# Optimization experiments

Measured on AMD Instinct MI355X. Metric: run time of the kernel, lower is better.

The kernel has to match this reference:

```python
import jax, jax.numpy as jnp
import numpy as np

H = 1024   # lstm hidden size
F = 512    # feature dim
P = 66     # pose dim
T_IN = 10
T_OUT = 25


def _glorot(key, shape):
    fan = shape[-1]
    return jax.random.normal(key, shape, dtype=jnp.float32) / np.sqrt(fan)


def setup_inputs() -> dict:
    key = jax.random.key(0)
    ks = jax.random.split(key, 24)
    B = 256
    inp = {
        'x': jax.random.normal(ks[0], (B, T_IN, P), dtype=jnp.float32),
        'z': jax.random.normal(ks[1], (B, T_IN, P), dtype=jnp.float32),
        'for_resid': jax.random.normal(ks[2], (B, T_OUT, P), dtype=jnp.float32),
        # ToFeature: Linear(66 -> 512)
        'tf_w': _glorot(ks[3], (F, P)), 'tf_b': jnp.zeros((F,), jnp.float32),
        # encoder LSTM(512 -> 1024)
        'enc_wih': _glorot(ks[4], (4 * H, F)), 'enc_whh': _glorot(ks[5], (4 * H, H)),
        'enc_bih': jnp.zeros((4 * H,), jnp.float32), 'enc_bhh': jnp.zeros((4 * H,), jnp.float32),
        # encoder_post LSTM(512 -> 1024)
        'encp_wih': _glorot(ks[6], (4 * H, F)), 'encp_whh': _glorot(ks[7], (4 * H, H)),
        'encp_bih': jnp.zeros((4 * H,), jnp.float32), 'encp_bhh': jnp.zeros((4 * H,), jnp.float32),
        # decoder cell LSTM(512 -> 1024)
        'dec_wih': _glorot(ks[8], (4 * H, F)), 'dec_whh': _glorot(ks[9], (4 * H, H)),
        'dec_bih': jnp.zeros((4 * H,), jnp.float32), 'dec_bhh': jnp.zeros((4 * H,), jnp.float32),
        # decoder lin: Linear(1024 -> 512)
        'lin_w': _glorot(ks[10], (F, H)), 'lin_b': jnp.zeros((F,), jnp.float32),
        # ToPose: Linear(1024 -> 66)
        'tp_w': _glorot(ks[11], (P, H)), 'tp_b': jnp.zeros((P,), jnp.float32),
    }
    return inp


def _lstm_step(h, c, xt, wih, whh, bih, bhh):
    gates = xt @ wih.T + bih + h @ whh.T + bhh  # (B, 4H)
    i, f, g, o = jnp.split(gates, 4, axis=-1)
    c_new = jax.nn.sigmoid(f) * c + jax.nn.sigmoid(i) * jnp.tanh(g)
    h_new = jax.nn.sigmoid(o) * jnp.tanh(c_new)
    return h_new, c_new


def _lstm_scan(xs, wih, whh, bih, bhh):
    # xs: (T, B, I)
    B = xs.shape[1]
    h0 = jnp.zeros((B, H), xs.dtype)
    c0 = jnp.zeros((B, H), xs.dtype)

    def step(carry, xt):
        h, c = carry
        h, c = _lstm_step(h, c, xt, wih, whh, bih, bhh)
        return (h, c), h

    (h_n, c_n), all_h = jax.lax.scan(step, (h0, c0), xs)
    return all_h, h_n, c_n


def reference(x, z, for_resid, tf_w, tf_b,
              enc_wih, enc_whh, enc_bih, enc_bhh,
              encp_wih, encp_whh, encp_bih, encp_bhh,
              dec_wih, dec_whh, dec_bih, dec_bhh,
              lin_w, lin_b, tp_w, tp_b):
    # ToFeature + permute to time-major (T, B, F)
    xf = jnp.transpose(x @ tf_w.T + tf_b, (1, 0, 2))
    zf = jnp.transpose(z @ tf_w.T + tf_b, (1, 0, 2))

    all_h, h_n, c_n = _lstm_scan(xf, enc_wih, enc_whh, enc_bih, enc_bhh)   # (10,B,H)
    all_hz, _, _ = _lstm_scan(zf, encp_wih, encp_whh, encp_bih, encp_bhh)  # (10,B,H)

    def dec_step(carry, _):
        h, c = carry                                   # (B,H), (B,H)
        cat_h = jnp.concatenate([all_h, h[None], all_hz], axis=0)  # (21,B,H)
        scores = jnp.einsum('bh,tbh->tb', c, cat_h)
        attw = jax.nn.softmax(scores, axis=0)
        atth = jnp.einsum('tb,tbh->bh', attw, cat_h)   # attention context -> LSTM h0
        inp = h @ lin_w.T + lin_b                      # (B,F)
        h_new, c_new = _lstm_step(atth, c, inp, dec_wih, dec_whh, dec_bih, dec_bhh)
        return (h_new, c_new), h_new

    _, dec_hs = jax.lax.scan(dec_step, (h_n, c_n), None, length=T_OUT)  # (25,B,H)
    out = jnp.transpose(dec_hs, (1, 0, 2))             # (B,25,H)
    o = out @ tp_w.T + tp_b                            # (B,25,66)
    return o + for_resid
```

## Files before the change

### kernel.cpp

```cpp
#include <hip/hip_runtime.h>
#include <hip/hip_bf16.h>
#include <hip/hip_cooperative_groups.h>

namespace cg = cooperative_groups;

#define DEV __device__ __forceinline__

typedef unsigned short u16;
typedef short bf16x8_t __attribute__((ext_vector_type(8)));
typedef float f32x4_t __attribute__((ext_vector_type(4)));

constexpr int NBLK = 256;
constexpr int NTHR = 512;
constexpr int NT_ALL = NBLK * NTHR;
constexpr size_t HSTRIDE = 256 * 1024;

struct Params {
  const float *x, *z, *resid, *tf_w, *tf_b;
  const float *e_wih, *e_whh, *e_bih, *e_bhh;
  const float *p_wih, *p_whh, *p_bih, *p_bhh;
  const float *d_wih, *d_whh, *d_bih, *d_bhh;
  const float *lin_w, *lin_b, *tp_w, *tp_b;
  u16 *Wenc, *Wencp, *Wdec, *wihP, *linT, *tpw;
  float *bias_e, *bias_ep, *bias_d, *bias_part;
  u16 *xf, *zf;
  u16 *he, *hp;
  u16 *hs;
  u16 *atth;
  float *c_pub;
  unsigned *bar;
  float *out;
};

DEV float b2f(u16 v) { unsigned u = ((unsigned)v) << 16; float f; __builtin_memcpy(&f, &u, 4); return f; }
DEV u16 f2b(float f) {
  unsigned u; __builtin_memcpy(&u, &f, 4);
  unsigned r = u + 0x7fffu + ((u >> 16) & 1u);
  return (u16)(r >> 16);
}
DEV unsigned pk2(float a, float b) { return (unsigned)f2b(a) | ((unsigned)f2b(b) << 16); }
DEV uint4 cvt8(const float* s) {
  float4 a = *(const float4*)s;
  float4 b = *(const float4*)(s + 4);
  uint4 r;
  r.x = pk2(a.x, a.y); r.y = pk2(a.z, a.w);
  r.z = pk2(b.x, b.y); r.w = pk2(b.z, b.w);
  return r;
}
DEV float sigm(float x) { return 1.0f / (1.0f + __expf(-x)); }
DEV f32x4_t fzero4() { f32x4_t v = {0.f, 0.f, 0.f, 0.f}; return v; }

DEV void gll16(const void* g, void* l) {
  __builtin_amdgcn_global_load_lds(
      (const __attribute__((address_space(1))) void*)g,
      (__attribute__((address_space(3))) void*)l, 16, 0, 0);
}

template <typename T> DEV void st_wt(T* p, T v) {
  __hip_atomic_store(p, v, __ATOMIC_RELAXED, __HIP_MEMORY_SCOPE_AGENT);
}
template <typename T> DEV T ld_byp(const T* p) {
  return __hip_atomic_load(p, __ATOMIC_RELAXED, __HIP_MEMORY_SCOPE_AGENT);
}

DEV void gridbar(unsigned* ctrs, unsigned ep, int tid, int bid) {
  asm volatile("s_waitcnt vmcnt(0)" ::: "memory");
  __syncthreads();
  if (tid == 0) atomicAdd(&ctrs[(bid & 7) * 16], 1u);
  if (tid < 8) {
    const unsigned tgt = ep * 32u;
    while (ld_byp(&ctrs[tid * 16]) < tgt) __builtin_amdgcn_s_sleep(2);
  }
  __syncthreads();
}
DEV void lanebar(unsigned* ctrs, unsigned ep, int lane, int j, int tid) {
  asm volatile("s_waitcnt vmcnt(0)" ::: "memory");
  __syncthreads();
  if (tid == 0) atomicAdd(&ctrs[(8 + lane * 2 + (j & 1)) * 16], 1u);
  if (tid < 2) {
    const unsigned tgt = ep * 32u;
    while (ld_byp(&ctrs[(8 + lane * 2 + tid) * 16]) < tgt) __builtin_amdgcn_s_sleep(1);
  }
  __syncthreads();
}

template <int PM>
DEV void gemm64(const u16* __restrict__ xa, int ldx, int xcols,
                const u16* __restrict__ ha, int ldh,
                const u16* __restrict__ wsrc, int ldw, int K,
                int m0, int n0, int tid, char* sm, f32x4_t acc[2]) {
  char* lB = sm;
  char* lA = sm + 32768;
  const int NK = K >> 6;
  const int row = tid >> 3, uu = tid & 7;
  const int usw = uu ^ (row & 7);
  const int wv = tid >> 6;
  char* la_base = lA + (wv << 10);
  char* lb_base = lB + (wv << 10);

  auto stageA = [&](int ks) {
    const int k0 = ks << 6;
    const u16* ga;
    if (k0 < xcols) ga = xa + (size_t)(m0 + row) * ldx + (k0 + usw * 8);
    else            ga = ha + (size_t)(m0 + row) * ldh + (k0 - xcols + usw * 8);
    gll16(ga, la_base + ((ks & 3) << 13));
  };
  auto stageB = [&](int ks) {
    const int k0 = ks << 6;
    const u16* gb = wsrc + (size_t)(n0 + row) * ldw + (k0 + usw * 8);
    gll16(gb, lb_base + ((ks & 3) << 13));
  };

  const int l = tid & 63, l15 = l & 15, lhi = l >> 4;
  const int wr = wv >> 1, wc = wv & 1;
  const int rA = wr * 16 + l15;
  const int aoff0 = rA * 128 + ((lhi ^ (rA & 7)) << 4);
  const int aoff1 = rA * 128 + (((lhi + 4) ^ (rA & 7)) << 4);
  const int nB0 = wc * 32 + l15, nB1 = nB0 + 16;
  const int boff00 = nB0 * 128 + ((lhi ^ (nB0 & 7)) << 4);
  const int boff01 = nB0 * 128 + (((lhi + 4) ^ (nB0 & 7)) << 4);
  const int boff10 = nB1 * 128 + ((lhi ^ (nB1 & 7)) << 4);
  const int boff11 = nB1 * 128 + (((lhi + 4) ^ (nB1 & 7)) << 4);

  if (PM == 0) { stageA(0); stageB(0); stageA(1); stageB(1); }
  if (PM == 2) { stageA(0); stageA(1); }

#pragma unroll 1
  for (int ks = 0; ks < NK; ++ks) {
    if (ks + 2 < NK) { stageA(ks + 2); stageB(ks + 2); }
    if (ks == 0)            asm volatile("s_waitcnt vmcnt(3)" ::: "memory");
    else if (ks + 2 < NK)   asm volatile("s_waitcnt vmcnt(4)" ::: "memory");
    else if (ks + 2 == NK)  asm volatile("s_waitcnt vmcnt(2)" ::: "memory");
    else                    asm volatile("s_waitcnt vmcnt(0)" ::: "memory");
    __builtin_amdgcn_s_barrier();
    const char* A  = lA + ((ks & 3) << 13);
    const char* Bb = lB + ((ks & 3) << 13);
    bf16x8_t a0  = *(const bf16x8_t*)(A + aoff0);
    bf16x8_t a1  = *(const bf16x8_t*)(A + aoff1);
    bf16x8_t b00 = *(const bf16x8_t*)(Bb + boff00);
    bf16x8_t b01 = *(const bf16x8_t*)(Bb + boff01);
    bf16x8_t b10 = *(const bf16x8_t*)(Bb + boff10);
    bf16x8_t b11 = *(const bf16x8_t*)(Bb + boff11);
    acc[0] = __builtin_amdgcn_mfma_f32_16x16x32_bf16(a0, b00, acc[0], 0, 0, 0);
    acc[0] = __builtin_amdgcn_mfma_f32_16x16x32_bf16(a1, b01, acc[0], 0, 0, 0);
    acc[1] = __builtin_amdgcn_mfma_f32_16x16x32_bf16(a0, b10, acc[1], 0, 0, 0);
    acc[1] = __builtin_amdgcn_mfma_f32_16x16x32_bf16(a1, b11, acc[1], 0, 0, 0);
  }
  __builtin_amdgcn_s_barrier();
}

DEV void pre_slotAB(const u16* xa, int ldx, int xcols, const u16* ha, int ldh,
                    const u16* wsrc, int ldw, int m0, int n0, int tid, char* sm,
                    int ks) {
  char* lB = sm; char* lA = sm + 32768;
  const int row = tid >> 3, uu = tid & 7;
  const int usw = uu ^ (row & 7);
  const int wv = tid >> 6;
  const int k0 = ks << 6;
  const u16* ga;
  if (k0 < xcols) ga = xa + (size_t)(m0 + row) * ldx + (k0 + usw * 8);
  else            ga = ha + (size_t)(m0 + row) * ldh + (k0 - xcols + usw * 8);
  const u16* gb = wsrc + (size_t)(n0 + row) * ldw + (k0 + usw * 8);
  gll16(ga, lA + (wv << 10) + ((ks & 3) << 13));
  gll16(gb, lB + (wv << 10) + ((ks & 3) << 13));
}
DEV void pre_slotB(const u16* wsrc, int ldw, int n0, int tid, char* sm, int ks) {
  char* lB = sm;
  const int row = tid >> 3, uu = tid & 7;
  const int usw = uu ^ (row & 7);
  const int wv = tid >> 6;
  const int k0 = ks << 6;
  const u16* gb = wsrc + (size_t)(n0 + row) * ldw + (k0 + usw * 8);
  gll16(gb, lB + (wv << 10) + ((ks & 3) << 13));
}

DEV void lstm_ep_reg(const f32x4_t acc[2], int tid, char* sm,
                     const float* __restrict__ bias, float cc[2],
                     u16* __restrict__ hw, float* __restrict__ cpub,
                     int m0, int n0) {
  float* gl = (float*)(sm + 49152);
  const int l = tid & 63, l15 = l & 15, lhi = l >> 4;
  const int wv = tid >> 6, wr = wv >> 1, wc = wv & 1;
#pragma unroll
  for (int j = 0; j < 2; ++j)
#pragma unroll
    for (int qq = 0; qq < 4; ++qq)
      gl[(wr * 16 + lhi * 4 + qq) * 64 + wc * 32 + j * 16 + l15] = acc[j][qq];
  __syncthreads();
#pragma unroll
  for (int it = 0; it < 2; ++it) {
    int idx = it * 512 + tid;
    int r = idx >> 4, jj = idx & 15;
    f32x4_t g4 = *(const f32x4_t*)(gl + r * 64 + jj * 4);
    f32x4_t b4 = *(const f32x4_t*)(bias + n0 + jj * 4);
    float ig = sigm(g4[0] + b4[0]);
    float fg = sigm(g4[1] + b4[1]);
    float g_ = tanhf(g4[2] + b4[2]);
    float og = sigm(g4[3] + b4[3]);
    float cn = fg * cc[it] + ig * g_;
    cc[it] = cn;
    float hn = og * tanhf(cn);
    size_t off = (size_t)(m0 + r) * 1024 + (n0 >> 2) + jj;
    st_wt(&hw[off], f2b(hn));
    if (cpub) st_wt(&cpub[off], cn);
  }
  __syncthreads();
}

DEV void wx_store(const f32x4_t acc[2], int tid, u16* __restrict__ Wdec,
                  int m0, int n0) {
  const int l = tid & 63, l15 = l & 15, lhi = l >> 4;
  const int wv = tid >> 6, wr = wv >> 1, wc = wv & 1;
#pragma unroll
  for (int j = 0; j < 2; ++j)
#pragma unroll
    for (int qq = 0; qq < 4; ++qq) {
      int r = m0 + wr * 16 + lhi * 4 + qq;
      int c = n0 + wc * 32 + j * 16 + l15;
      st_wt(&Wdec[(size_t)r * 2048 + c], f2b(acc[j][qq]));
    }
}

DEV void phase0_tf(const Params& p, int bid, int tid, char* sm) {
  float* xs = (float*)sm;
  float* zs = (float*)(sm + 2688);
  for (int g = tid; g < 660; g += NTHR) {
    int t = g / 66, q = g - t * 66;
    xs[g] = p.x[((size_t)bid * 10 + t) * 66 + q];
    zs[g] = p.z[((size_t)bid * 10 + t) * 66 + q];
  }
  __syncthreads();
  const int n = tid;
  float accx[10], accz[10];
  float bn = p.tf_b[n];
#pragma unroll
  for (int t = 0; t < 10; ++t) { accx[t] = bn; accz[t] = bn; }
  const float* wrow = p.tf_w + (size_t)n * 66;
  for (int k = 0; k < 66; ++k) {
    float wk = wrow[k];
#pragma unroll
    for (int t = 0; t < 10; ++t) {
      accx[t] = fmaf(wk, xs[t * 66 + k], accx[t]);
      accz[t] = fmaf(wk, zs[t * 66 + k], accz[t]);
    }
  }
#pragma unroll
  for (int t = 0; t < 10; ++t) {
    p.xf[(size_t)t * 131072 + (size_t)bid * 512 + n] = f2b(accx[t]);
    p.zf[(size_t)t * 131072 + (size_t)bid * 512 + n] = f2b(accz[t]);
  }
  __syncthreads();
}

DEV void phase0a(const Params& p, int gtid) {
  for (int g = gtid; g < 786432; g += NT_ALL) {
    int row = g / 192;
    int u = g - row * 192;
    int k = u * 8;
    int nsrc = (row & 3) * 1024 + (row >> 2);
    const float* s1 = (k < 512) ? (p.e_wih + (size_t)nsrc * 512 + k)
                                : (p.e_whh + (size_t)nsrc * 1024 + (k - 512));
    ((uint4*)p.Wenc)[g] = cvt8(s1);
    const float* s2 = (k < 512) ? (p.p_wih + (size_t)nsrc * 512 + k)
                                : (p.p_whh + (size_t)nsrc * 1024 + (k - 512));
    ((uint4*)p.Wencp)[g] = cvt8(s2);
  }
  for (int g = gtid; g < 524288; g += NT_ALL) {
    int row = g >> 7, u = g & 127;
    int nsrc = (row & 3) * 1024 + (row >> 2);
    ((uint4*)p.Wdec)[row * 256 + 128 + u] = cvt8(p.d_whh + (size_t)nsrc * 1024 + u * 8);
  }
  for (int g = gtid; g < 262144; g += NT_ALL) {
    int row = g >> 6, u = g & 63;
    int nsrc = (row & 3) * 1024 + (row >> 2);
    ((uint4*)p.wihP)[g] = cvt8(p.d_wih + (size_t)nsrc * 512 + u * 8);
  }
  for (int g = gtid; g < 524288; g += NT_ALL) {
    int f = g >> 10, h = g & 1023;
    p.linT[(size_t)h * 512 + f] = f2b(p.lin_w[g]);
  }
  for (int g = gtid; g < 8448; g += NT_ALL)
    ((uint4*)p.tpw)[g] = cvt8(p.tp_w + g * 8);
  for (int g = gtid; g < 4096; g += NT_ALL) {
    int nsrc = (g & 3) * 1024 + (g >> 2);
    p.bias_e[g]  = p.e_bih[nsrc] + p.e_bhh[nsrc];
    p.bias_ep[g] = p.p_bih[nsrc] + p.p_bhh[nsrc];
  }
  for (int g = gtid; g < 32768; g += NT_ALL) {
    int cell = g >> 3, sub = g & 7;
    int nsrc = (cell & 3) * 1024 + (cell >> 2);
    const float* wr_ = p.d_wih + (size_t)nsrc * 512 + sub * 64;
    const float* lb = p.lin_b + sub * 64;
    float s = 0.f;
    for (int f = 0; f < 64; ++f) s += wr_[f] * lb[f];
    p.bias_part[g] = s;
  }
  uint4 zz; zz.x = zz.y = zz.z = zz.w = 0u;
  for (int g = gtid; g < 32768; g += NT_ALL) { ((uint4*)p.he)[g] = zz; ((uint4*)p.hp)[g] = zz; }
}

DEV void attention(const Params& p, const u16* hd_prev, const float* cpub,
                   u16* atth_s, int b, int tid, char* sm) {
  u16*   catl = (u16*)(sm + 16384);
  float* cl   = (float*)(sm + 59392);
  float* sc   = (float*)(sm + 63488);
  for (int g = tid; g < 2688; g += NTHR) {
    int t = g >> 7, hu = g & 127;
    const u16* src;
    if (t < 10)       src = p.he + (size_t)(t + 1) * HSTRIDE;
    else if (t == 10) src = hd_prev;
    else              src = p.hp + (size_t)(t - 10) * HSTRIDE;
    ((uint4*)catl)[g] = *(const uint4*)(src + (size_t)b * 1024 + hu * 8);
  }
  for (int g = tid; g < 512; g += NTHR) {
    unsigned long long v = ld_byp(((const unsigned long long*)(cpub + (size_t)b * 1024)) + g);
    ((unsigned long long*)cl)[g] = v;
  }
  __syncthreads();
  const int wv = tid >> 6, l = tid & 63;
  for (int t = wv; t < 21; t += 8) {
    float s = 0.f;
    const u16* cr = catl + t * 1024;
    for (int hh = l; hh < 1024; hh += 64) s += cl[hh] * b2f(cr[hh]);
#pragma unroll
    for (int o = 32; o; o >>= 1) s += __shfl_down(s, o);
    if (l == 0) sc[t] = s;
  }
  __syncthreads();
  float m = -1e30f;
#pragma unroll
  for (int t = 0; t < 21; ++t) m = fmaxf(m, sc[t]);
  float e[21]; float den = 0.f;
#pragma unroll
  for (int t = 0; t < 21; ++t) { e[t] = __expf(sc[t] - m); den += e[t]; }
  float inv = 1.0f / den;
  const int h0 = tid * 2;
  float a0 = 0.f, a1 = 0.f;
#pragma unroll
  for (int t = 0; t < 21; ++t) {
    float w_ = e[t] * inv;
    unsigned v = *(const unsigned*)(catl + t * 1024 + h0);
    a0 += w_ * b2f((u16)(v & 0xffff));
    a1 += w_ * b2f((u16)(v >> 16));
  }
  st_wt(((unsigned*)(atth_s + (size_t)b * 1024)) + tid, pk2(a0, a1));
  __syncthreads();
}

DEV void finalproj(const Params& p, int b, int tid, char* sm) {
  u16* hl = (u16*)sm;
  for (int g = tid; g < 3200; g += NTHR) {
    int t = g >> 7, hu = g & 127;
    ((uint4*)hl)[g] = *(const uint4*)(p.hs + ((size_t)(t * 256 + b)) * 1024 + hu * 8);
  }
  __syncthreads();
  if (tid < 330) {
    int pcol = tid % 66, tg = tid / 66;
    float acc[5] = {0.f, 0.f, 0.f, 0.f, 0.f};
    const u16* wrow = p.tpw + (size_t)pcol * 1024;
    for (int hc = 0; hc < 128; ++hc) {
      uint4 wv4 = ((const uint4*)wrow)[hc];
      float wf[8];
      wf[0] = b2f(wv4.x & 0xffff); wf[1] = b2f(wv4.x >> 16);
      wf[2] = b2f(wv4.y & 0xffff); wf[3] = b2f(wv4.y >> 16);
      wf[4] = b2f(wv4.z & 0xffff); wf[5] = b2f(wv4.z >> 16);
      wf[6] = b2f(wv4.w & 0xffff); wf[7] = b2f(wv4.w >> 16);
#pragma unroll
      for (int r = 0; r < 5; ++r) {
        int t = tg * 5 + r;
        uint4 hv = ((const uint4*)(hl + t * 1024))[hc];
        float s;
        s  = wf[0] * b2f(hv.x & 0xffff) + wf[1] * b2f(hv.x >> 16);
        s += wf[2] * b2f(hv.y & 0xffff) + wf[3] * b2f(hv.y >> 16);
        s += wf[4] * b2f(hv.z & 0xffff) + wf[5] * b2f(hv.z >> 16);
        s += wf[6] * b2f(hv.w & 0xffff) + wf[7] * b2f(hv.w >> 16);
        acc[r] += s;
      }
    }
    float bb = p.tp_b[pcol];
#pragma unroll
    for (int r = 0; r < 5; ++r) {
      int t = tg * 5 + r;
      size_t o = (size_t)b * 1650 + (size_t)t * 66 + pcol;
      p.out[o] = acc[r] + bb + p.resid[o];
    }
  }
}

__global__ __launch_bounds__(NTHR) void model_kernel(Params p) {
  cg::grid_group gg = cg::this_grid();
  __shared__ __align__(16) char sm[65536];
  const int tid = threadIdx.x;
  const int bid = blockIdx.x;
  const int gtid = bid * NTHR + tid;

  phase0_tf(p, bid, tid, sm);
  phase0a(p, gtid);
  if (bid == 0 && tid < 16) st_wt(&p.bar[tid * 16], 0u);
  gg.sync();

  for (int g = gtid; g < 4096; g += NT_ALL) {
    int nsrc = (g & 3) * 1024 + (g >> 2);
    float s = p.d_bih[nsrc] + p.d_bhh[nsrc];
#pragma unroll
    for (int k8 = 0; k8 < 8; ++k8) s += p.bias_part[g * 8 + k8];
    st_wt(&p.bias_d[g], s);
  }
#pragma unroll 1
  for (int i = 0; i < 4; ++i) {
    int tt = bid * 4 + i;
    int m0w = (tt & 63) << 6;
    int n0w = (tt >> 6) << 6;
    f32x4_t acc[2]; acc[0] = fzero4(); acc[1] = fzero4();
    gemm64<0>(p.wihP, 512, 512, p.wihP, 0, p.linT, 512, 512, m0w, n0w, tid, sm, acc);
    wx_store(acc, tid, p.Wdec, m0w, n0w);
  }

  const int lane = bid >> 6, j = bid & 63;
  const int m0 = lane << 6;
  const int n0 = ((j & 7) * 8 + (j >> 3)) << 6;
  const int b = (lane << 6) + j;

  pre_slotAB(p.xf, 512, 512, p.he, 1024, p.Wenc, 1536, m0, n0, tid, sm, 0);
  pre_slotAB(p.xf, 512, 512, p.he, 1024, p.Wenc, 1536, m0, n0, tid, sm, 1);
  gridbar(p.bar, 1, tid, bid);

  float ce[2] = {0.f, 0.f}, cp[2] = {0.f, 0.f};
  unsigned lep = 0;

#pragma unroll 1
  for (int t = 0; t < 10; ++t) {
    f32x4_t acc[2]; acc[0] = fzero4(); acc[1] = fzero4();
    gemm64<1>(p.xf + (size_t)t * 131072, 512, 512, p.he + (size_t)t * HSTRIDE, 1024,
              p.Wenc, 1536, 1536, m0, n0, tid, sm, acc);
    pre_slotAB(p.zf + (size_t)t * 131072, 512, 512, p.hp, 1024, p.Wencp, 1536, m0, n0, tid, sm, 0);
    pre_slotAB(p.zf + (size_t)t * 131072, 512, 512, p.hp, 1024, p.Wencp, 1536, m0, n0, tid, sm, 1);
    lstm_ep_reg(acc, tid, sm, p.bias_e, ce, p.he + (size_t)(t + 1) * HSTRIDE,
                (t == 9) ? p.c_pub : (float*)0, m0, n0);
    acc[0] = fzero4(); acc[1] = fzero4();
    gemm64<1>(p.zf + (size_t)t * 131072, 512, 512, p.hp + (size_t)t * HSTRIDE, 1024,
              p.Wencp, 1536, 1536, m0, n0, tid, sm, acc);
    if (t < 9) {
      pre_slotAB(p.xf + (size_t)(t + 1) * 131072, 512, 512, p.he, 1024, p.Wenc, 1536, m0, n0, tid, sm, 0);
      pre_slotAB(p.xf + (size_t)(t + 1) * 131072, 512, 512, p.he, 1024, p.Wenc, 1536, m0, n0, tid, sm, 1);
    } else {
      pre_slotB(p.Wdec, 2048, n0, tid, sm, 0);
      pre_slotB(p.Wdec, 2048, n0, tid, sm, 1);
    }
    lstm_ep_reg(acc, tid, sm, p.bias_ep, cp, p.hp + (size_t)(t + 1) * HSTRIDE,
                (float*)0, m0, n0);
    ++lep; lanebar(p.bar, lep, lane, j, tid);
  }

#pragma unroll 1
  for (int s = 0; s < 25; ++s) {
    const u16* hd_prev = (s == 0) ? (p.he + (size_t)10 * HSTRIDE)
                                  : (p.hs + (size_t)(s - 1) * HSTRIDE);
    u16* atth_s = p.atth + (size_t)s * HSTRIDE;
    attention(p, hd_prev, p.c_pub + (size_t)(s & 1) * 262144, atth_s, b, tid, sm);
    f32x4_t acc[2]; acc[0] = fzero4(); acc[1] = fzero4();
    gemm64<2>(hd_prev, 1024, 1024, hd_prev, 1024, p.Wdec, 2048, 1024,
              m0, n0, tid, sm, acc);
    pre_slotB(p.Wdec + 1024, 2048, n0, tid, sm, 0);
    pre_slotB(p.Wdec + 1024, 2048, n0, tid, sm, 1);
    ++lep; lanebar(p.bar, lep, lane, j, tid);
    gemm64<2>(atth_s, 1024, 1024, atth_s, 1024, p.Wdec + 1024, 2048, 1024,
              m0, n0, tid, sm, acc);
    lstm_ep_reg(acc, tid, sm, p.bias_d, ce, p.hs + (size_t)s * HSTRIDE,
                p.c_pub + (size_t)((s + 1) & 1) * 262144, m0, n0);
    if (s < 24) {
      pre_slotB(p.Wdec, 2048, n0, tid, sm, 0);
      pre_slotB(p.Wdec, 2048, n0, tid, sm, 1);
    }
    ++lep; lanebar(p.bar, lep, lane, j, tid);
  }

  finalproj(p, b, tid, sm);
}

extern "C" void kernel_launch(void* const* d_in, const int* in_sizes, int n_in,
                              void* d_out, int out_size, void* d_ws, size_t ws_size,
                              hipStream_t stream) {
  (void)in_sizes; (void)n_in; (void)out_size;
  Params P;
  P.x     = (const float*)d_in[0];
  P.z     = (const float*)d_in[1];
  P.resid = (const float*)d_in[2];
  P.tf_w  = (const float*)d_in[3];
  P.tf_b  = (const float*)d_in[4];
  P.e_wih = (const float*)d_in[5];
  P.e_whh = (const float*)d_in[6];
  P.e_bih = (const float*)d_in[7];
  P.e_bhh = (const float*)d_in[8];
  P.p_wih = (const float*)d_in[9];
  P.p_whh = (const float*)d_in[10];
  P.p_bih = (const float*)d_in[11];
  P.p_bhh = (const float*)d_in[12];
  P.d_wih = (const float*)d_in[13];
  P.d_whh = (const float*)d_in[14];
  P.d_bih = (const float*)d_in[15];
  P.d_bhh = (const float*)d_in[16];
  P.lin_w = (const float*)d_in[17];
  P.lin_b = (const float*)d_in[18];
  P.tp_w  = (const float*)d_in[19];
  P.tp_b  = (const float*)d_in[20];

  char* w = (char*)d_ws;
  size_t o = 0;
  auto take = [&](size_t bytes) { char* r = w + o; o = (o + bytes + 255) & ~(size_t)255; return r; };
  P.Wenc  = (u16*)take(4096ull * 1536 * 2);
  P.Wencp = (u16*)take(4096ull * 1536 * 2);
  P.Wdec  = (u16*)take(4096ull * 2048 * 2);
  P.wihP  = (u16*)take(4096ull * 512 * 2);
  P.linT  = (u16*)take(1024ull * 512 * 2);
  P.tpw   = (u16*)take(66ull * 1024 * 2);
  P.bias_e    = (float*)take(4096 * 4);
  P.bias_ep   = (float*)take(4096 * 4);
  P.bias_d    = (float*)take(4096 * 4);
  P.bias_part = (float*)take(32768 * 4);
  P.xf  = (u16*)take(10ull * 256 * 512 * 2);
  P.zf  = (u16*)take(10ull * 256 * 512 * 2);
  P.he  = (u16*)take(11ull * 256 * 1024 * 2);
  P.hp  = (u16*)take(11ull * 256 * 1024 * 2);
  P.hs  = (u16*)take(25ull * 256 * 1024 * 2);
  P.atth = (u16*)take(25ull * 256 * 1024 * 2);
  P.c_pub = (float*)take(2ull * 256 * 1024 * 4);
  P.bar = (unsigned*)take(16 * 64);
  P.out = (float*)d_out;

  if (o > ws_size) return;

  void* args[] = { &P };
  hipLaunchCooperativeKernel((const void*)model_kernel, dim3(NBLK, 1, 1),
                             dim3(NTHR, 1, 1), args, 0, stream);
}
```

Measured before the change: 815.1 us.

## Load weight tiles directly into registers and stage only activations through LDS

The GEMM now loads the weight (B) fragments straight from global memory into registers with an even/odd double buffer, and stages only the activation (A) operand through LDS. The cross-phase weight prefetches into LDS are removed, and lane barriers now spread arrivals over 8 counters instead of 2. LDS becomes dynamic with a padded epilogue layout. This is meant to cut LDS traffic and barrier contention, but it loses the prefetch overlap across phases and adds register pressure.

```diff
diff --git a/kernel.cpp b/kernel.cpp
--- a/kernel.cpp
+++ b/kernel.cpp
@@ -14,6 +14,7 @@
 constexpr int NTHR = 512;
 constexpr int NT_ALL = NBLK * NTHR;
 constexpr size_t HSTRIDE = 256 * 1024;
+constexpr int SMEM_BYTES = 86016;
 
 struct Params {
   const float *x, *z, *resid, *tf_w, *tf_b;
@@ -63,135 +64,114 @@
   return __hip_atomic_load(p, __ATOMIC_RELAXED, __HIP_MEMORY_SCOPE_AGENT);
 }
 
-DEV void gridbar(unsigned* ctrs, unsigned ep, int tid, int bid) {
+DEV void fullbar(unsigned* ctrs, int bid, unsigned tgt, int tid) {
   asm volatile("s_waitcnt vmcnt(0)" ::: "memory");
   __syncthreads();
   if (tid == 0) atomicAdd(&ctrs[(bid & 7) * 16], 1u);
-  if (tid < 8) {
-    const unsigned tgt = ep * 32u;
-    while (ld_byp(&ctrs[tid * 16]) < tgt) __builtin_amdgcn_s_sleep(2);
-  }
-  __syncthreads();
-}
-DEV void lanebar(unsigned* ctrs, unsigned ep, int lane, int j, int tid) {
+  if (tid < 8) { while (ld_byp(&ctrs[tid * 16]) < tgt) __builtin_amdgcn_s_sleep(2); }
+  __syncthreads();
+}
+DEV void lanebar8(unsigned* ctrs, int lane, int j, unsigned tgt, int tid) {
   asm volatile("s_waitcnt vmcnt(0)" ::: "memory");
   __syncthreads();
-  if (tid == 0) atomicAdd(&ctrs[(8 + lane * 2 + (j & 1)) * 16], 1u);
-  if (tid < 2) {
-    const unsigned tgt = ep * 32u;
-    while (ld_byp(&ctrs[(8 + lane * 2 + tid) * 16]) < tgt) __builtin_amdgcn_s_sleep(1);
-  }
-  __syncthreads();
-}
-
-template <int PM>
-DEV void gemm64(const u16* __restrict__ xa, int ldx, int xcols,
-                const u16* __restrict__ ha, int ldh,
-                const u16* __restrict__ wsrc, int ldw, int K,
-                int m0, int n0, int tid, char* sm, f32x4_t acc[2]) {
-  char* lB = sm;
-  char* lA = sm + 32768;
+  if (tid == 0) atomicAdd(&ctrs[(8 + lane * 8 + (j & 7)) * 16], 1u);
+  if (tid < 8) { while (ld_byp(&ctrs[(8 + lane * 8 + tid) * 16]) < tgt) __builtin_amdgcn_s_sleep(1); }
+  __syncthreads();
+}
+
+struct Bpre { bf16x8_t e00, e01, e10, e11, o00, o01, o10, o11; };
+
+DEV void gemmT(const u16* __restrict__ xa, int ldx, int xcols,
+               const u16* __restrict__ ha, int ldh,
+               const u16* __restrict__ w, int ldw, int K,
+               int m0, int n0, int tid, char* sm, f32x4_t acc[2]) {
+  Bpre B;
   const int NK = K >> 6;
-  const int row = tid >> 3, uu = tid & 7;
-  const int usw = uu ^ (row & 7);
-  const int wv = tid >> 6;
-  char* la_base = lA + (wv << 10);
-  char* lb_base = lB + (wv << 10);
-
-  auto stageA = [&](int ks) {
-    const int k0 = ks << 6;
-    const u16* ga;
-    if (k0 < xcols) ga = xa + (size_t)(m0 + row) * ldx + (k0 + usw * 8);
-    else            ga = ha + (size_t)(m0 + row) * ldh + (k0 - xcols + usw * 8);
-    gll16(ga, la_base + ((ks & 3) << 13));
-  };
-  auto stageB = [&](int ks) {
-    const int k0 = ks << 6;
-    const u16* gb = wsrc + (size_t)(n0 + row) * ldw + (k0 + usw * 8);
-    gll16(gb, lb_base + ((ks & 3) << 13));
-  };
-
-  const int l = tid & 63, l15 = l & 15, lhi = l >> 4;
-  const int wr = wv >> 1, wc = wv & 1;
-  const int rA = wr * 16 + l15;
+  const int row = tid >> 3, usw8 = ((tid & 7) ^ (row & 7)) * 8, wv = tid >> 6;
+  char* dst = sm + (wv << 10);
+  const u16* aX = xa + (size_t)(m0 + row) * ldx + usw8;
+  const u16* aH = ha + (size_t)(m0 + row) * ldh + usw8 - xcols;
+  const int wc = (tid >> 6) & 1, l15 = tid & 15, lhi = (tid & 63) >> 4;
+  const u16* pb0 = w + (size_t)(n0 + wc * 32 + l15) * ldw + lhi * 8;
+  const u16* pb1 = pb0 + (size_t)16 * ldw;
+  const int rA = (tid >> 7) * 16 + l15;
   const int aoff0 = rA * 128 + ((lhi ^ (rA & 7)) << 4);
   const int aoff1 = rA * 128 + (((lhi + 4) ^ (rA & 7)) << 4);
-  const int nB0 = wc * 32 + l15, nB1 = nB0 + 16;
-  const int boff00 = nB0 * 128 + ((lhi ^ (nB0 & 7)) << 4);
-  const int boff01 = nB0 * 128 + (((lhi + 4) ^ (nB0 & 7)) << 4);
-  const int boff10 = nB1 * 128 + ((lhi ^ (nB1 & 7)) << 4);
-  const int boff11 = nB1 * 128 + (((lhi + 4) ^ (nB1 & 7)) << 4);
-
-  if (PM == 0) { stageA(0); stageB(0); stageA(1); stageB(1); }
-  if (PM == 2) { stageA(0); stageA(1); }
-
+
+  auto sA = [&](int ks) {
+    const int k0 = ks << 6;
+    const u16* g = (k0 < xcols) ? (aX + k0) : (aH + k0);
+    gll16(g, dst + ((ks & 3) << 13));
+  };
+  auto ldE = [&](int ks) {
+    const int k0 = ks << 6;
+    B.e00 = *(const bf16x8_t*)(pb0 + k0);
+    B.e01 = *(const bf16x8_t*)(pb0 + k0 + 32);
+    B.e10 = *(const bf16x8_t*)(pb1 + k0);
+    B.e11 = *(const bf16x8_t*)(pb1 + k0 + 32);
+  };
+  auto ldO = [&](int ks) {
+    const int k0 = ks << 6;
+    B.o00 = *(const bf16x8_t*)(pb0 + k0);
+    B.o01 = *(const bf16x8_t*)(pb0 + k0 + 32);
+    B.o10 = *(const bf16x8_t*)(pb1 + k0);
+    B.o11 = *(const bf16x8_t*)(pb1 + k0 + 32);
+  };
+
+  sA(0); ldE(0); sA(1); ldO(1);
+
+  auto body = [&](int ks, bool useE, int wN, bool issue) {
+    if (wN == 5) asm volatile("s_waitcnt vmcnt(5)" ::: "memory");
+    else         asm volatile("s_waitcnt vmcnt(0)" ::: "memory");
+    __builtin_amdgcn_sched_barrier(0);
+    __builtin_amdgcn_s_barrier();
+    __builtin_amdgcn_sched_barrier(0);
+    const char* Asl = sm + ((ks & 3) << 13);
+    bf16x8_t a0 = *(const bf16x8_t*)(Asl + aoff0);
+    bf16x8_t a1 = *(const bf16x8_t*)(Asl + aoff1);
+    if (useE) {
+      acc[0] = __builtin_amdgcn_mfma_f32_16x16x32_bf16(a0, B.e00, acc[0], 0, 0, 0);
+      acc[0] = __builtin_amdgcn_mfma_f32_16x16x32_bf16(a1, B.e01, acc[0], 0, 0, 0);
+      acc[1] = __builtin_amdgcn_mfma_f32_16x16x32_bf16(a0, B.e10, acc[1], 0, 0, 0);
+      acc[1] = __builtin_amdgcn_mfma_f32_16x16x32_bf16(a1, B.e11, acc[1], 0, 0, 0);
+    } else {
+      acc[0] = __builtin_amdgcn_mfma_f32_16x16x32_bf16(a0, B.o00, acc[0], 0, 0, 0);
+      acc[0] = __builtin_amdgcn_mfma_f32_16x16x32_bf16(a1, B.o01, acc[0], 0, 0, 0);
+      acc[1] = __builtin_amdgcn_mfma_f32_16x16x32_bf16(a0, B.o10, acc[1], 0, 0, 0);
+      acc[1] = __builtin_amdgcn_mfma_f32_16x16x32_bf16(a1, B.o11, acc[1], 0, 0, 0);
+    }
+    if (issue) { sA(ks + 2); if (useE) ldE(ks + 2); else ldO(ks + 2); }
+  };
+
+  body(0, true, 5, true);
+  body(1, false, 5, true);
 #pragma unroll 1
-  for (int ks = 0; ks < NK; ++ks) {
-    if (ks + 2 < NK) { stageA(ks + 2); stageB(ks + 2); }
-    if (ks == 0)            asm volatile("s_waitcnt vmcnt(3)" ::: "memory");
-    else if (ks + 2 < NK)   asm volatile("s_waitcnt vmcnt(4)" ::: "memory");
-    else if (ks + 2 == NK)  asm volatile("s_waitcnt vmcnt(2)" ::: "memory");
-    else                    asm volatile("s_waitcnt vmcnt(0)" ::: "memory");
-    __builtin_amdgcn_s_barrier();
-    const char* A  = lA + ((ks & 3) << 13);
-    const char* Bb = lB + ((ks & 3) << 13);
-    bf16x8_t a0  = *(const bf16x8_t*)(A + aoff0);
-    bf16x8_t a1  = *(const bf16x8_t*)(A + aoff1);
-    bf16x8_t b00 = *(const bf16x8_t*)(Bb + boff00);
-    bf16x8_t b01 = *(const bf16x8_t*)(Bb + boff01);
-    bf16x8_t b10 = *(const bf16x8_t*)(Bb + boff10);
-    bf16x8_t b11 = *(const bf16x8_t*)(Bb + boff11);
-    acc[0] = __builtin_amdgcn_mfma_f32_16x16x32_bf16(a0, b00, acc[0], 0, 0, 0);
-    acc[0] = __builtin_amdgcn_mfma_f32_16x16x32_bf16(a1, b01, acc[0], 0, 0, 0);
-    acc[1] = __builtin_amdgcn_mfma_f32_16x16x32_bf16(a0, b10, acc[1], 0, 0, 0);
-    acc[1] = __builtin_amdgcn_mfma_f32_16x16x32_bf16(a1, b11, acc[1], 0, 0, 0);
-  }
-  __builtin_amdgcn_s_barrier();
-}
-
-DEV void pre_slotAB(const u16* xa, int ldx, int xcols, const u16* ha, int ldh,
-                    const u16* wsrc, int ldw, int m0, int n0, int tid, char* sm,
-                    int ks) {
-  char* lB = sm; char* lA = sm + 32768;
-  const int row = tid >> 3, uu = tid & 7;
-  const int usw = uu ^ (row & 7);
-  const int wv = tid >> 6;
-  const int k0 = ks << 6;
-  const u16* ga;
-  if (k0 < xcols) ga = xa + (size_t)(m0 + row) * ldx + (k0 + usw * 8);
-  else            ga = ha + (size_t)(m0 + row) * ldh + (k0 - xcols + usw * 8);
-  const u16* gb = wsrc + (size_t)(n0 + row) * ldw + (k0 + usw * 8);
-  gll16(ga, lA + (wv << 10) + ((ks & 3) << 13));
-  gll16(gb, lB + (wv << 10) + ((ks & 3) << 13));
-}
-DEV void pre_slotB(const u16* wsrc, int ldw, int n0, int tid, char* sm, int ks) {
-  char* lB = sm;
-  const int row = tid >> 3, uu = tid & 7;
-  const int usw = uu ^ (row & 7);
-  const int wv = tid >> 6;
-  const int k0 = ks << 6;
-  const u16* gb = wsrc + (size_t)(n0 + row) * ldw + (k0 + usw * 8);
-  gll16(gb, lB + (wv << 10) + ((ks & 3) << 13));
-}
-
-DEV void lstm_ep_reg(const f32x4_t acc[2], int tid, char* sm,
-                     const float* __restrict__ bias, float cc[2],
-                     u16* __restrict__ hw, float* __restrict__ cpub,
-                     int m0, int n0) {
-  float* gl = (float*)(sm + 49152);
-  const int l = tid & 63, l15 = l & 15, lhi = l >> 4;
+  for (int ks = 2; ks < NK - 2; ks += 2) {
+    body(ks, true, 5, true);
+    body(ks + 1, false, 5, true);
+  }
+  body(NK - 2, true, 5, false);
+  body(NK - 1, false, 0, false);
+}
+
+DEV void lstm_ep(const f32x4_t acc[2], int tid, char* sm,
+                 const float* __restrict__ bias, float cc[2],
+                 u16* __restrict__ hw, float* __restrict__ cpub,
+                 int m0, int n0) {
+  float* gl = (float*)(sm + 32768);
+  const int l15 = tid & 15, lhi = (tid & 63) >> 4;
   const int wv = tid >> 6, wr = wv >> 1, wc = wv & 1;
 #pragma unroll
-  for (int j = 0; j < 2; ++j)
+  for (int jf = 0; jf < 2; ++jf)
 #pragma unroll
     for (int qq = 0; qq < 4; ++qq)
-      gl[(wr * 16 + lhi * 4 + qq) * 64 + wc * 32 + j * 16 + l15] = acc[j][qq];
+      gl[(wr * 16 + lhi * 4 + qq) * 68 + wc * 32 + jf * 16 + l15] = acc[jf][qq];
   __syncthreads();
 #pragma unroll
   for (int it = 0; it < 2; ++it) {
     int idx = it * 512 + tid;
     int r = idx >> 4, jj = idx & 15;
-    f32x4_t g4 = *(const f32x4_t*)(gl + r * 64 + jj * 4);
+    f32x4_t g4 = *(const f32x4_t*)(gl + r * 68 + jj * 4);
     f32x4_t b4 = *(const f32x4_t*)(bias + n0 + jj * 4);
     float ig = sigm(g4[0] + b4[0]);
     float fg = sigm(g4[1] + b4[1]);
@@ -209,15 +189,15 @@
 
 DEV void wx_store(const f32x4_t acc[2], int tid, u16* __restrict__ Wdec,
                   int m0, int n0) {
-  const int l = tid & 63, l15 = l & 15, lhi = l >> 4;
+  const int l15 = tid & 15, lhi = (tid & 63) >> 4;
   const int wv = tid >> 6, wr = wv >> 1, wc = wv & 1;
 #pragma unroll
-  for (int j = 0; j < 2; ++j)
+  for (int jf = 0; jf < 2; ++jf)
 #pragma unroll
     for (int qq = 0; qq < 4; ++qq) {
       int r = m0 + wr * 16 + lhi * 4 + qq;
-      int c = n0 + wc * 32 + j * 16 + l15;
-      st_wt(&Wdec[(size_t)r * 2048 + c], f2b(acc[j][qq]));
+      int c = n0 + wc * 32 + jf * 16 + l15;
+      st_wt(&Wdec[(size_t)r * 2048 + c], f2b(acc[jf][qq]));
     }
 }
 
@@ -225,9 +205,9 @@
   float* xs = (float*)sm;
   float* zs = (float*)(sm + 2688);
   for (int g = tid; g < 660; g += NTHR) {
-    int t = g / 66, q = g - t * 66;
-    xs[g] = p.x[((size_t)bid * 10 + t) * 66 + q];
-    zs[g] = p.z[((size_t)bid * 10 + t) * 66 + q];
+    int t = g / 66, qd = g - t * 66;
+    xs[g] = p.x[((size_t)bid * 10 + t) * 66 + qd];
+    zs[g] = p.z[((size_t)bid * 10 + t) * 66 + qd];
   }
   __syncthreads();
   const int n = tid;
@@ -301,9 +281,9 @@
 
 DEV void attention(const Params& p, const u16* hd_prev, const float* cpub,
                    u16* atth_s, int b, int tid, char* sm) {
-  u16*   catl = (u16*)(sm + 16384);
-  float* cl   = (float*)(sm + 59392);
-  float* sc   = (float*)(sm + 63488);
+  u16*   catl = (u16*)(sm + 32768);
+  float* cl   = (float*)(sm + 75776);
+  float* sc   = (float*)(sm + 79872);
   for (int g = tid; g < 2688; g += NTHR) {
     int t = g >> 7, hu = g & 127;
     const u16* src;
@@ -348,7 +328,7 @@
 }
 
 DEV void finalproj(const Params& p, int b, int tid, char* sm) {
-  u16* hl = (u16*)sm;
+  u16* hl = (u16*)(sm + 32768);
   for (int g = tid; g < 3200; g += NTHR) {
     int t = g >> 7, hu = g & 127;
     ((uint4*)hl)[g] = *(const uint4*)(p.hs + ((size_t)(t * 256 + b)) * 1024 + hu * 8);
@@ -389,14 +369,14 @@
 
 __global__ __launch_bounds__(NTHR) void model_kernel(Params p) {
   cg::grid_group gg = cg::this_grid();
-  __shared__ __align__(16) char sm[65536];
+  extern __shared__ __align__(16) char sm[];
   const int tid = threadIdx.x;
   const int bid = blockIdx.x;
   const int gtid = bid * NTHR + tid;
 
   phase0_tf(p, bid, tid, sm);
   phase0a(p, gtid);
-  if (bid == 0 && tid < 16) st_wt(&p.bar[tid * 16], 0u);
+  if (bid == 0 && tid < 40) st_wt(&p.bar[tid * 16], 0u);
   gg.sync();
 
   for (int g = gtid; g < 4096; g += NT_ALL) {
@@ -406,24 +386,23 @@
     for (int k8 = 0; k8 < 8; ++k8) s += p.bias_part[g * 8 + k8];
     st_wt(&p.bias_d[g], s);
   }
+
 #pragma unroll 1
   for (int i = 0; i < 4; ++i) {
     int tt = bid * 4 + i;
     int m0w = (tt & 63) << 6;
     int n0w = (tt >> 6) << 6;
     f32x4_t acc[2]; acc[0] = fzero4(); acc[1] = fzero4();
-    gemm64<0>(p.wihP, 512, 512, p.wihP, 0, p.linT, 512, 512, m0w, n0w, tid, sm, acc);
+    gemmT(p.wihP, 512, 512, p.wihP, 512, p.linT, 512, 512,
+          m0w, n0w, tid, sm, acc);
     wx_store(acc, tid, p.Wdec, m0w, n0w);
   }
 
   const int lane = bid >> 6, j = bid & 63;
   const int m0 = lane << 6;
   const int n0 = ((j & 7) * 8 + (j >> 3)) << 6;
-  const int b = (lane << 6) + j;
-
-  pre_slotAB(p.xf, 512, 512, p.he, 1024, p.Wenc, 1536, m0, n0, tid, sm, 0);
-  pre_slotAB(p.xf, 512, 512, p.he, 1024, p.Wenc, 1536, m0, n0, tid, sm, 1);
-  gridbar(p.bar, 1, tid, bid);
+
+  fullbar(p.bar, bid, 32u, tid);
 
   float ce[2] = {0.f, 0.f}, cp[2] = {0.f, 0.f};
   unsigned lep = 0;
@@ -431,25 +410,16 @@
 #pragma unroll 1
   for (int t = 0; t < 10; ++t) {
     f32x4_t acc[2]; acc[0] = fzero4(); acc[1] = fzero4();
-    gemm64<1>(p.xf + (size_t)t * 131072, 512, 512, p.he + (size_t)t * HSTRIDE, 1024,
-              p.Wenc, 1536, 1536, m0, n0, tid, sm, acc);
-    pre_slotAB(p.zf + (size_t)t * 131072, 512, 512, p.hp, 1024, p.Wencp, 1536, m0, n0, tid, sm, 0);
-    pre_slotAB(p.zf + (size_t)t * 131072, 512, 512, p.hp, 1024, p.Wencp, 1536, m0, n0, tid, sm, 1);
-    lstm_ep_reg(acc, tid, sm, p.bias_e, ce, p.he + (size_t)(t + 1) * HSTRIDE,
-                (t == 9) ? p.c_pub : (float*)0, m0, n0);
+    gemmT(p.xf + (size_t)t * 131072, 512, 512, p.he + (size_t)t * HSTRIDE, 1024,
+          p.Wenc, 1536, 1536, m0, n0, tid, sm, acc);
+    lstm_ep(acc, tid, sm, p.bias_e, ce, p.he + (size_t)(t + 1) * HSTRIDE,
+            (t == 9) ? p.c_pub : (float*)0, m0, n0);
     acc[0] = fzero4(); acc[1] = fzero4();
-    gemm64<1>(p.zf + (size_t)t * 131072, 512, 512, p.hp + (size_t)t * HSTRIDE, 1024,
-              p.Wencp, 1536, 1536, m0, n0, tid, sm, acc);
-    if (t < 9) {
-      pre_slotAB(p.xf + (size_t)(t + 1) * 131072, 512, 512, p.he, 1024, p.Wenc, 1536, m0, n0, tid, sm, 0);
-      pre_slotAB(p.xf + (size_t)(t + 1) * 131072, 512, 512, p.he, 1024, p.Wenc, 1536, m0, n0, tid, sm, 1);
-    } else {
-      pre_slotB(p.Wdec, 2048, n0, tid, sm, 0);
-      pre_slotB(p.Wdec, 2048, n0, tid, sm, 1);
-    }
-    lstm_ep_reg(acc, tid, sm, p.bias_ep, cp, p.hp + (size_t)(t + 1) * HSTRIDE,
-                (float*)0, m0, n0);
-    ++lep; lanebar(p.bar, lep, lane, j, tid);
+    gemmT(p.zf + (size_t)t * 131072, 512, 512, p.hp + (size_t)t * HSTRIDE, 1024,
+          p.Wencp, 1536, 1536, m0, n0, tid, sm, acc);
+    lstm_ep(acc, tid, sm, p.bias_ep, cp, p.hp + (size_t)(t + 1) * HSTRIDE,
+            (float*)0, m0, n0);
+    ++lep; lanebar8(p.bar, lane, j, lep * 8u, tid);
   }
 
 #pragma unroll 1
@@ -457,25 +427,19 @@
     const u16* hd_prev = (s == 0) ? (p.he + (size_t)10 * HSTRIDE)
                                   : (p.hs + (size_t)(s - 1) * HSTRIDE);
     u16* atth_s = p.atth + (size_t)s * HSTRIDE;
-    attention(p, hd_prev, p.c_pub + (size_t)(s & 1) * 262144, atth_s, b, tid, sm);
+    attention(p, hd_prev, p.c_pub + (size_t)(s & 1) * 262144, atth_s, bid, tid, sm);
     f32x4_t acc[2]; acc[0] = fzero4(); acc[1] = fzero4();
-    gemm64<2>(hd_prev, 1024, 1024, hd_prev, 1024, p.Wdec, 2048, 1024,
-              m0, n0, tid, sm, acc);
-    pre_slotB(p.Wdec + 1024, 2048, n0, tid, sm, 0);
-    pre_slotB(p.Wdec + 1024, 2048, n0, tid, sm, 1);
-    ++lep; lanebar(p.bar, lep, lane, j, tid);
-    gemm64<2>(atth_s, 1024, 1024, atth_s, 1024, p.Wdec + 1024, 2048, 1024,
-              m0, n0, tid, sm, acc);
-    lstm_ep_reg(acc, tid, sm, p.bias_d, ce, p.hs + (size_t)s * HSTRIDE,
-                p.c_pub + (size_t)((s + 1) & 1) * 262144, m0, n0);
-    if (s < 24) {
-      pre_slotB(p.Wdec, 2048, n0, tid, sm, 0);
-      pre_slotB(p.Wdec, 2048, n0, tid, sm, 1);
-    }
-    ++lep; lanebar(p.bar, lep, lane, j, tid);
-  }
-
-  finalproj(p, b, tid, sm);
+    gemmT(hd_prev, 1024, 1024, hd_prev, 1024, p.Wdec, 2048, 1024,
+          m0, n0, tid, sm, acc);
+    ++lep; lanebar8(p.bar, lane, j, lep * 8u, tid);
+    gemmT(atth_s, 1024, 1024, atth_s, 1024, p.Wdec + 1024, 2048, 1024,
+          m0, n0, tid, sm, acc);
+    lstm_ep(acc, tid, sm, p.bias_d, ce, p.hs + (size_t)s * HSTRIDE,
+            p.c_pub + (size_t)((s + 1) & 1) * 262144, m0, n0);
+    ++lep; lanebar8(p.bar, lane, j, lep * 8u, tid);
+  }
+
+  finalproj(p, bid, tid, sm);
 }
 
 extern "C" void kernel_launch(void* const* d_in, const int* in_sizes, int n_in,
@@ -525,12 +489,15 @@
   P.hs  = (u16*)take(25ull * 256 * 1024 * 2);
   P.atth = (u16*)take(25ull * 256 * 1024 * 2);
   P.c_pub = (float*)take(2ull * 256 * 1024 * 4);
-  P.bar = (unsigned*)take(16 * 64);
+  P.bar   = (unsigned*)take(40 * 64);
   P.out = (float*)d_out;
 
   if (o > ws_size) return;
+
+  hipFuncSetAttribute((const void*)model_kernel,
+                      hipFuncAttributeMaxDynamicSharedMemorySize, SMEM_BYTES);
 
   void* args[] = { &P };
   hipLaunchCooperativeKernel((const void*)model_kernel, dim3(NBLK, 1, 1),
-                             dim3(NTHR, 1, 1), args, 0, stream);
-}
+                             dim3(NTHR, 1, 1), args, SMEM_BYTES, stream);
+}
```

New measurement: 1.660 ms. 104% more time.
